# Optimization experiments

Hardware: AMD Instinct MI355X
Metric: run time of the kernel (lower is better)

The kernel has to match this reference:

```python
import jax, jax.numpy as jnp
import numpy as np

N_NODES = 100000
N_EDGES = 3200000
D_FEAT = 128


def setup_inputs() -> dict:
    key = jax.random.key(0)
    k1, k2, k3, k4 = jax.random.split(key, 4)
    edge_row = jax.random.randint(k1, (N_EDGES,), 0, N_NODES)
    edge_col = jax.random.randint(k2, (N_EDGES,), 0, N_NODES)
    edge_val = jax.random.uniform(k3, (N_EDGES,), dtype=jnp.float32)
    embs = jax.random.normal(k4, (N_NODES, D_FEAT), dtype=jnp.float32)
    return {
        "edge_row": edge_row,
        "edge_col": edge_col,
        "edge_val": edge_val,
        "embs": embs,
        "n_nodes": N_NODES,
    }


def reference(edge_row, edge_col, edge_val, embs, n_nodes):
    # out[r] = sum_{e: row[e]==r} val[e] * embs[col[e]]  == (sparse adj) @ embs
    msgs = embs[edge_col] * edge_val[:, None]  # [E, D] gather + scale
    return jax.ops.segment_sum(msgs, edge_row, num_segments=n_nodes)  # [N, D]
```

## Files before the change

kernel.cpp:

```cpp
#include <hip/hip_runtime.h>
#include <hip/hip_fp16.h>


#define D_FEAT 128
#define CSHIFT 9
#define CROWS 512
#define MAXNBC 256
#define PAD 16
#define BLK1 256
#define EPT1 16
#define EPB1 (BLK1 * EPT1)
#define BLK2 1024

__device__ __forceinline__ int wave_incl_scan(int x, int lane) {
#pragma unroll
    for (int off = 1; off < 64; off <<= 1) {
        int y = __shfl_up(x, off, 64);
        if (lane >= off) x += y;
    }
    return x;
}

__global__ __launch_bounds__(BLK1) void k_part1conv(const int* __restrict__ row,
                                                    const int* __restrict__ col,
                                                    const float* __restrict__ val,
                                                    int* __restrict__ gcur,
                                                    int2* __restrict__ tmp1,
                                                    int n_edges, int nbc, int slot,
                                                    int nchunks,
                                                    const float* __restrict__ embs,
                                                    __half* __restrict__ embs16,
                                                    int n_units16) {
    int tid = threadIdx.x;
    if ((int)blockIdx.x >= nchunks) {
        int i = (blockIdx.x - nchunks) * BLK1 + tid;
        if (i >= n_units16) return;
        const float4* src = reinterpret_cast<const float4*>(embs) + (size_t)i * 4;
        float4 f0 = src[0];
        float4 f1 = src[1];
        float4 f2 = src[2];
        float4 f3 = src[3];
        __half2* dst = reinterpret_cast<__half2*>(embs16) + (size_t)i * 8;
        dst[0] = __floats2half2_rn(f0.x, f0.y);
        dst[1] = __floats2half2_rn(f0.z, f0.w);
        dst[2] = __floats2half2_rn(f1.x, f1.y);
        dst[3] = __floats2half2_rn(f1.z, f1.w);
        dst[4] = __floats2half2_rn(f2.x, f2.y);
        dst[5] = __floats2half2_rn(f2.z, f2.w);
        dst[6] = __floats2half2_rn(f3.x, f3.y);
        dst[7] = __floats2half2_rn(f3.z, f3.w);
        return;
    }
    __shared__ int2 stage[EPB1];
    __shared__ int lcnt[MAXNBC], lstart[257], lcur[MAXNBC];
    __shared__ int lbase[MAXNBC], lroom[MAXNBC];
    __shared__ int wsum[4];
    int lane = tid & 63, wid = tid >> 6;
    for (int j = tid; j < nbc; j += BLK1) { lcnt[j] = 0; lcur[j] = 0; }
    __syncthreads();

    int base = blockIdx.x * EPB1;
    int ne = n_edges - base; if (ne > EPB1) ne = EPB1;

    int r[EPT1], c[EPT1]; float v[EPT1];
#pragma unroll
    for (int k = 0; k < EPT1; ++k) {
        int e = base + k * BLK1 + tid;
        r[k] = -1;
        if (e < n_edges) {
            r[k] = row[e]; c[k] = col[e]; v[k] = val[e];
            atomicAdd(&lcnt[r[k] >> CSHIFT], 1);
        }
    }
    __syncthreads();
    int cv = (tid < nbc) ? lcnt[tid] : 0;
    int incl = wave_incl_scan(cv, lane);
    if (lane == 63) wsum[wid] = incl;
    __syncthreads();
    if (tid < 4) {
        int w = wsum[tid];
        int ss = w;
#pragma unroll
        for (int off = 1; off < 4; off <<= 1) {
            int y = __shfl_up(ss, off, 64);
            if (tid >= off) ss += y;
        }
        wsum[tid] = ss - w;
    }
    __syncthreads();
    int ex = wsum[wid] + incl - cv;
    lstart[tid] = (tid < nbc) ? ex : ne;
    if (tid == BLK1 - 1) lstart[256] = ne;
    if (tid < nbc && cv) {
        int res = atomicAdd(&gcur[tid * PAD], cv);
        lbase[tid] = tid * slot + res;
        lroom[tid] = slot - res;
    }
    __syncthreads();
    if (tid == 0 && nbc < 256) lstart[nbc] = ne;
    __syncthreads();
#pragma unroll
    for (int k = 0; k < EPT1; ++k) {
        if (r[k] >= 0) {
            int b = r[k] >> CSHIFT;
            int sl = lstart[b] + atomicAdd(&lcur[b], 1);
            stage[sl] = make_int2(((r[k] & (CROWS - 1)) << 17) | c[k],
                                  __float_as_int(v[k]));
        }
    }
    __syncthreads();
#define P1_SEARCH_STORE(ii)                                                \
    {                                                                      \
        int _i = (ii);                                                     \
        int lo = 0;                                                        \
        lo += (lstart[lo + 128] <= _i) ? 128 : 0;                          \
        lo += (lstart[lo + 64]  <= _i) ? 64  : 0;                          \
        lo += (lstart[lo + 32]  <= _i) ? 32  : 0;                          \
        lo += (lstart[lo + 16]  <= _i) ? 16  : 0;                          \
        lo += (lstart[lo + 8]   <= _i) ? 8   : 0;                          \
        lo += (lstart[lo + 4]   <= _i) ? 4   : 0;                          \
        lo += (lstart[lo + 2]   <= _i) ? 2   : 0;                          \
        lo += (lstart[lo + 1]   <= _i) ? 1   : 0;                          \
        int off = _i - lstart[lo];                                         \
        if (off < lroom[lo])   \
            tmp1[lbase[lo] + off] = stage[_i];                             \
    }
    if (ne == EPB1) {
#pragma unroll 4
        for (int k = 0; k < EPT1; ++k) P1_SEARCH_STORE(k * BLK1 + tid);
    } else {
        for (int i = tid; i < ne; i += BLK1) P1_SEARCH_STORE(i);
    }
#undef P1_SEARCH_STORE
}

__global__ __launch_bounds__(BLK2) void k_p2(const int2* __restrict__ tmp1,
                                             const int* __restrict__ gcur,
                                             int2* __restrict__ pcv,
                                             int* __restrict__ row_start,
                                             int* __restrict__ row_cnt,
                                             int n_nodes, int nbc, int slot) {
    __shared__ int rcnt[CROWS], rstart[CROWS], rcur[CROWS];
    __shared__ int wsum[8];
    __shared__ int s[256];
    int b = blockIdx.x, tid = threadIdx.x;
    int lane = tid & 63, wid = tid >> 6;

    if (tid < 256) {
        int c = (tid < nbc) ? gcur[tid * PAD] : 0;
        s[tid] = (c > slot) ? slot : c;
    }
    __syncthreads();
    for (int off = 1; off < 256; off <<= 1) {
        int u = (tid < 256 && tid >= off) ? s[tid - off] : 0;
        __syncthreads();
        if (tid < 256) s[tid] += u;
        __syncthreads();
    }
    int cnt = gcur[b * PAD]; if (cnt > slot) cnt = slot;
    int pbase = s[b] - cnt;
    const int2* src = tmp1 + (size_t)b * slot;

    for (int j = tid; j < CROWS; j += BLK2) { rcnt[j] = 0; rcur[j] = 0; }
    __syncthreads();
    for (int i = tid; i < cnt; i += BLK2)
        atomicAdd(&rcnt[((unsigned)src[i].x) >> 17], 1);
    __syncthreads();
    int v = (tid < CROWS) ? rcnt[tid] : 0;
    int incl = wave_incl_scan(v, lane);
    if (lane == 63 && wid < 8) wsum[wid] = incl;
    __syncthreads();
    if (tid < 8) {
        int w = wsum[tid];
        int ss = w;
#pragma unroll
        for (int off = 1; off < 8; off <<= 1) {
            int y = __shfl_up(ss, off, 64);
            if (tid >= off) ss += y;
        }
        wsum[tid] = ss - w;
    }
    __syncthreads();
    if (tid < CROWS) rstart[tid] = wsum[wid] + incl - v;
    __syncthreads();
    if (tid < CROWS) {
        int gr = (b << CSHIFT) + tid;
        if (gr < n_nodes) {
            row_start[gr] = pbase + rstart[tid];
            row_cnt[gr]   = v;
        }
    }
    for (int i = tid; i < cnt; i += BLK2) {
        int2 p = src[i];
        int lr = ((unsigned)p.x) >> 17;
        int pos = pbase + rstart[lr] + atomicAdd(&rcur[lr], 1);
        pcv[pos] = make_int2(p.x & 0x1FFFF, p.y);
    }
}

__global__ __launch_bounds__(256) void k_rows_h(const int2* __restrict__ pcv,
                                                const int* __restrict__ row_start,
                                                const int* __restrict__ row_cnt,
                                                const __half2* __restrict__ eb,
                                                float* __restrict__ out, int n_nodes) {
    int gtid = blockIdx.x * blockDim.x + threadIdx.x;
    int r = gtid >> 6;
    int lane = threadIdx.x & 63;
    if (r >= n_nodes) return;

    int start = row_start[r];
    int end   = start + row_cnt[r];

    float2 acc = make_float2(0.f, 0.f);

    int i = start;
    for (; i + 8 <= end; i += 8) {
        int2 p[8];
#pragma unroll
        for (int k = 0; k < 8; ++k) p[k] = pcv[i + k];
        __half2 h[8];
#pragma unroll
        for (int k = 0; k < 8; ++k) h[k] = eb[(size_t)p[k].x * 64 + lane];
#pragma unroll
        for (int k = 0; k < 8; ++k) {
            float v = __int_as_float(p[k].y);
            float2 f = __half22float2(h[k]);
            acc.x += v * f.x;
            acc.y += v * f.y;
        }
    }
    for (; i < end; ++i) {
        int2 p = pcv[i];
        float v = __int_as_float(p.y);
        float2 f = __half22float2(eb[(size_t)p.x * 64 + lane]);
        acc.x += v * f.x;
        acc.y += v * f.y;
    }
    reinterpret_cast<float2*>(out)[(size_t)r * 64 + lane] = acc;
}

__global__ void gcn_scatter_atomic(const int* __restrict__ edge_row,
                                   const int* __restrict__ edge_col,
                                   const float* __restrict__ edge_val,
                                   const float* __restrict__ embs,
                                   float* __restrict__ out, int n_edges) {
    long long tid = (long long)blockIdx.x * blockDim.x + threadIdx.x;
    int sub = (int)(tid & 31);
    long long edge = tid >> 5;
    if (edge >= n_edges) return;
    int r = edge_row[edge];
    int c = edge_col[edge];
    float v = edge_val[edge];
    const float4* src = reinterpret_cast<const float4*>(embs + (size_t)c * D_FEAT);
    float4 m = src[sub];
    float* dst = out + (size_t)r * D_FEAT + (size_t)sub * 4;
    atomicAdd(dst + 0, m.x * v);
    atomicAdd(dst + 1, m.y * v);
    atomicAdd(dst + 2, m.z * v);
    atomicAdd(dst + 3, m.w * v);
}

extern "C" void kernel_launch(void* const* d_in, const int* in_sizes, int n_in,
                              void* d_out, int out_size, void* d_ws, size_t ws_size,
                              hipStream_t stream) {
    const int*   edge_row = (const int*)d_in[0];
    const int*   edge_col = (const int*)d_in[1];
    const float* edge_val = (const float*)d_in[2];
    const float* embs     = (const float*)d_in[3];
    float*       out      = (float*)d_out;

    const int n_edges = in_sizes[0];
    const int n_nodes = out_size / D_FEAT;
    const int nbc = (n_nodes + CROWS - 1) >> CSHIFT;

    const int avg = (n_edges + nbc - 1) / nbc;
    const int slot = (avg + (avg >> 2) + 2048 + 63) & ~63;

    char* ws = (char*)d_ws;
    const size_t off_pcv       = 0;
    const size_t off_row_start = off_pcv + (size_t)n_edges * 8;
    const size_t off_row_cnt   = off_row_start + (size_t)n_nodes * 4;
    const size_t off_gcur      = off_row_cnt + (size_t)n_nodes * 4;
    const size_t off_embs16    = off_gcur + (size_t)MAXNBC * PAD * 4;
    const size_t full_ws       = off_embs16 + (size_t)n_nodes * D_FEAT * 2;

    bool tmp_fits = ((size_t)nbc * slot * 8 <= (size_t)out_size * 4);
    bool packs_ok = (n_nodes <= 131072) && (nbc <= MAXNBC) &&
                    ((n_nodes * D_FEAT) % 16 == 0);

    if (ws_size < full_ws || !tmp_fits || !packs_ok) {
        hipMemsetAsync(d_out, 0, (size_t)out_size * sizeof(float), stream);
        long long total = (long long)n_edges * 32;
        int blocks = (int)((total + 255) / 256);
        gcn_scatter_atomic<<<blocks, 256, 0, stream>>>(edge_row, edge_col, edge_val,
                                                       embs, out, n_edges);
        return;
    }

    int2*   pcv       = (int2*)(ws + off_pcv);
    int*    row_start = (int*)(ws + off_row_start);
    int*    row_cnt   = (int*)(ws + off_row_cnt);
    int*    gcur      = (int*)(ws + off_gcur);
    __half* embs16    = (__half*)(ws + off_embs16);
    int2*   tmp1      = (int2*)d_out;

    hipMemsetAsync(gcur, 0, (size_t)MAXNBC * PAD * 4, stream);

    const int nchunks = (n_edges + EPB1 - 1) / EPB1;
    const int n_units16 = n_nodes * (D_FEAT / 16);
    const int conv_blocks = (n_units16 + BLK1 - 1) / BLK1;

    k_part1conv<<<nchunks + conv_blocks, BLK1, 0, stream>>>(
        edge_row, edge_col, edge_val, gcur, tmp1, n_edges, nbc, slot,
        nchunks, embs, embs16, n_units16);
    k_p2<<<nbc, BLK2, 0, stream>>>(tmp1, gcur, pcv, row_start, row_cnt,
                                   n_nodes, nbc, slot);

    long long rows_threads = (long long)n_nodes * 64;
    int rblocks = (int)((rows_threads + 255) / 256);
    k_rows_h<<<rblocks, 256, 0, stream>>>(pcv, row_start, row_cnt,
                                          (const __half2*)embs16, out, n_nodes);
}
```

Measured before the change: 300.6 us.

## Split second partition pass across four blocks per bucket by row subrange

The second sort pass now launches four blocks per coarse bucket instead of one. Each block still reads the whole bucket, builds the full row histogram and scan, but scatters only the edges whose local row falls in its quarter of the 512-row range, using a smaller shared cursor array. The aim is more parallelism and less shared-atomic contention during the scatter. The cost is four times the reads of the bucket data and redundant histogram work.

```diff
diff --git a/kernel.cpp b/kernel.cpp
--- a/kernel.cpp
+++ b/kernel.cpp
@@ -11,6 +11,7 @@
 #define EPT1 16
 #define EPB1 (BLK1 * EPT1)
 #define BLK2 1024
+#define NS2 4
 
 __device__ __forceinline__ int wave_incl_scan(int x, int lane) {
 #pragma unroll
@@ -140,28 +141,33 @@
                                              int* __restrict__ row_start,
                                              int* __restrict__ row_cnt,
                                              int n_nodes, int nbc, int slot) {
-    __shared__ int rcnt[CROWS], rstart[CROWS], rcur[CROWS];
+    __shared__ int rcnt[CROWS], rstart[CROWS], rcur[CROWS / NS2];
     __shared__ int wsum[8];
-    __shared__ int s[256];
-    int b = blockIdx.x, tid = threadIdx.x;
+    __shared__ int sc[256];
+    int b = blockIdx.x >> 2;
+    int sl2 = blockIdx.x & (NS2 - 1);
+    int tid = threadIdx.x;
     int lane = tid & 63, wid = tid >> 6;
+    const int rlo = sl2 * (CROWS / NS2);
+    const int rhi = rlo + (CROWS / NS2);
 
     if (tid < 256) {
         int c = (tid < nbc) ? gcur[tid * PAD] : 0;
-        s[tid] = (c > slot) ? slot : c;
+        sc[tid] = (c > slot) ? slot : c;
     }
     __syncthreads();
     for (int off = 1; off < 256; off <<= 1) {
-        int u = (tid < 256 && tid >= off) ? s[tid - off] : 0;
+        int u = (tid < 256 && tid >= off) ? sc[tid - off] : 0;
         __syncthreads();
-        if (tid < 256) s[tid] += u;
+        if (tid < 256) sc[tid] += u;
         __syncthreads();
     }
     int cnt = gcur[b * PAD]; if (cnt > slot) cnt = slot;
-    int pbase = s[b] - cnt;
+    int pbase = sc[b] - cnt;
     const int2* src = tmp1 + (size_t)b * slot;
 
-    for (int j = tid; j < CROWS; j += BLK2) { rcnt[j] = 0; rcur[j] = 0; }
+    for (int j = tid; j < CROWS; j += BLK2) rcnt[j] = 0;
+    if (tid < CROWS / NS2) rcur[tid] = 0;
     __syncthreads();
     for (int i = tid; i < cnt; i += BLK2)
         atomicAdd(&rcnt[((unsigned)src[i].x) >> 17], 1);
@@ -183,7 +189,7 @@
     __syncthreads();
     if (tid < CROWS) rstart[tid] = wsum[wid] + incl - v;
     __syncthreads();
-    if (tid < CROWS) {
+    if (tid >= rlo && tid < rhi) {
         int gr = (b << CSHIFT) + tid;
         if (gr < n_nodes) {
             row_start[gr] = pbase + rstart[tid];
@@ -193,8 +199,10 @@
     for (int i = tid; i < cnt; i += BLK2) {
         int2 p = src[i];
         int lr = ((unsigned)p.x) >> 17;
-        int pos = pbase + rstart[lr] + atomicAdd(&rcur[lr], 1);
-        pcv[pos] = make_int2(p.x & 0x1FFFF, p.y);
+        if (lr >= rlo && lr < rhi) {
+            int pos = pbase + rstart[lr] + atomicAdd(&rcur[lr - rlo], 1);
+            pcv[pos] = make_int2(p.x & 0x1FFFF, p.y);
+        }
     }
 }
 
@@ -313,8 +321,8 @@
     k_part1conv<<<nchunks + conv_blocks, BLK1, 0, stream>>>(
         edge_row, edge_col, edge_val, gcur, tmp1, n_edges, nbc, slot,
         nchunks, embs, embs16, n_units16);
-    k_p2<<<nbc, BLK2, 0, stream>>>(tmp1, gcur, pcv, row_start, row_cnt,
-                                   n_nodes, nbc, slot);
+    k_p2<<<nbc * NS2, BLK2, 0, stream>>>(tmp1, gcur, pcv, row_start, row_cnt,
+                                         n_nodes, nbc, slot);
 
     long long rows_threads = (long long)n_nodes * 64;
     int rblocks = (int)((rows_threads + 255) / 256);
```

Measured after the change: 317.4 us. +5.6%, slower.
